# Performance work log

Hardware: AMD Instinct MI355X
Metric: run time of the kernel (lower is better)

The kernel has to match this reference:

```python
import jax, jax.numpy as jnp
import numpy as np


def setup_inputs() -> dict:
    key = jax.random.key(0)
    k_x, k_wih, k_whh, k_bih, k_bhh = jax.random.split(key, 5)
    B, T, F, H = 64, 2048, 256, 512
    s = 1.0 / np.sqrt(H)  # PyTorch RNN default init scale
    return {
        "query": jax.random.normal(k_x, (B, T, F), dtype=jnp.float32),
        "W_ih": jax.random.uniform(k_wih, (H, F), jnp.float32, -s, s),
        "W_hh": jax.random.uniform(k_whh, (H, H), jnp.float32, -s, s),
        "b_ih": jax.random.uniform(k_bih, (H,), jnp.float32, -s, s),
        "b_hh": jax.random.uniform(k_bhh, (H,), jnp.float32, -s, s),
    }


def reference(query, W_ih, W_hh, b_ih, b_hh):
    # Vanilla tanh RNN (batch_first): h_t = tanh(x_t W_ih^T + b_ih + h_{t-1} W_hh^T + b_hh)
    B, T, F = query.shape
    H = W_hh.shape[0]
    # Precompute the input projection for all timesteps as one big GEMM.
    x_proj = jnp.einsum("btf,hf->bth", query, W_ih) + b_ih + b_hh  # [B, T, H]

    def step(h, x_t):
        h_new = jnp.tanh(x_t + h @ W_hh.T)  # [B, H]
        return h_new, h_new

    h0 = jnp.zeros((B, H), dtype=query.dtype)
    h_last, outs = jax.lax.scan(step, h0, jnp.swapaxes(x_proj, 0, 1))  # scan over T
    output = jnp.swapaxes(outs, 0, 1)  # [B, T, H]
    hidden = h_last[None]              # [1, B, H] (num_layers=1)
    return output, hidden
```

## Files before the change

### kernel.cpp

```cpp
#include <hip/hip_runtime.h>
#include <cstdint>

#define B_SZ 64
#define T_SZ 2048
#define F_SZ 256
#define H_SZ 512

typedef _Float16 f16x8 __attribute__((ext_vector_type(8)));
typedef float f32x4 __attribute__((ext_vector_type(4)));

#if defined(__has_builtin)
#if __has_builtin(__builtin_amdgcn_fdot2)
#define HAVE_FDOT2 1
#endif
#endif
#ifndef HAVE_FDOT2
#define HAVE_FDOT2 0
#endif

typedef _Float16 half2v __attribute__((ext_vector_type(2)));
union H2U { uint32_t u; half2v h; _Float16 e[2]; };

__device__ __forceinline__ float fdot2f(uint32_t a, uint32_t b, float c) {
  H2U ua, ub; ua.u = a; ub.u = b;
#if HAVE_FDOT2
  return __builtin_amdgcn_fdot2(ua.h, ub.h, c, false);
#else
  return c + (float)ua.e[0] * (float)ub.e[0] + (float)ua.e[1] * (float)ub.e[1];
#endif
}

__device__ __forceinline__ uint32_t pack2h(float x, float y) {
  H2U v; v.e[0] = (_Float16)x; v.e[1] = (_Float16)y; return v.u;
}

__device__ __forceinline__ float fast_tanh(float x) {
  float xc = fminf(9.0f, fmaxf(-9.0f, x));
  float e = __expf(2.0f * xc);
  return (e - 1.0f) / (e + 1.0f);
}

__device__ __forceinline__ f16x8 pack8(const float* p) {
  float4 v0 = *(const float4*)p;
  float4 v1 = *(const float4*)(p + 4);
  f16x8 a;
  a[0] = (_Float16)v0.x; a[1] = (_Float16)v0.y;
  a[2] = (_Float16)v0.z; a[3] = (_Float16)v0.w;
  a[4] = (_Float16)v1.x; a[5] = (_Float16)v1.y;
  a[6] = (_Float16)v1.z; a[7] = (_Float16)v1.w;
  return a;
}

__device__ __forceinline__ void step_barrier() {
  asm volatile("s_waitcnt lgkmcnt(0)\n\ts_barrier" ::: "memory");
}

__global__ __launch_bounds__(512) void prep_kernel(
    const float* __restrict__ w_hh, uint4* __restrict__ wsf) {
  int idx = blockIdx.x * 512 + threadIdx.x;
  int lane = idx & 63;
  int kt = (idx >> 6) & 15;
  int w = idx >> 10;
  int m = lane & 15, g = lane >> 4;
  const float* p = w_hh + (size_t)(64 * w + 48 + m) * H_SZ + kt * 32 + g * 8;
  f16x8 a = pack8(p);
  wsf[idx] = __builtin_bit_cast(uint4, a);
}

__global__ __launch_bounds__(256) void proj_kernel(
    const float* __restrict__ q, const float* __restrict__ w_ih,
    const float* __restrict__ b_ih, const float* __restrict__ b_hh,
    float* __restrict__ xp) {
  __shared__ uint32_t lds_a[16][128 + 4];
  __shared__ uint32_t lds_b[16][128 + 4];
  const int tid = threadIdx.x;
  const int nt = blockIdx.x & 3;
  const int mt = blockIdx.x >> 2;
  const int m0 = mt * 128, n0 = nt * 128;
  const int tx = tid & 15, ty = tid >> 4;
  const int sr = tid >> 3, sc4 = tid & 7;

  float bias[8];
#pragma unroll
  for (int j = 0; j < 8; ++j) {
    int n = n0 + tx * 8 + j;
    bias[j] = b_ih[n] + b_hh[n];
  }
  float acc[8][8];
#pragma unroll
  for (int i = 0; i < 8; ++i)
#pragma unroll
    for (int j = 0; j < 8; ++j) acc[i][j] = 0.f;

  for (int k0 = 0; k0 < F_SZ; k0 += 32) {
#pragma unroll
    for (int i = 0; i < 4; ++i) {
      int r = sr + 32 * i;
      float4 v = *(const float4*)(q + (size_t)(m0 + r) * F_SZ + k0 + sc4 * 4);
      lds_a[sc4 * 2 + 0][r] = pack2h(v.x, v.y);
      lds_a[sc4 * 2 + 1][r] = pack2h(v.z, v.w);
      float4 w = *(const float4*)(w_ih + (size_t)(n0 + r) * F_SZ + k0 + sc4 * 4);
      lds_b[sc4 * 2 + 0][r] = pack2h(w.x, w.y);
      lds_b[sc4 * 2 + 1][r] = pack2h(w.z, w.w);
    }
    __syncthreads();
#pragma unroll
    for (int kp = 0; kp < 16; ++kp) {
      uint32_t a8[8], b8[8];
#pragma unroll
      for (int i = 0; i < 8; ++i) a8[i] = lds_a[kp][ty * 8 + i];
#pragma unroll
      for (int j = 0; j < 8; ++j) b8[j] = lds_b[kp][tx * 8 + j];
#pragma unroll
      for (int i = 0; i < 8; ++i)
#pragma unroll
        for (int j = 0; j < 8; ++j)
          acc[i][j] = fdot2f(a8[i], b8[j], acc[i][j]);
    }
    __syncthreads();
  }
#pragma unroll
  for (int i = 0; i < 8; ++i) {
    size_t row = (size_t)(m0 + ty * 8 + i);
    float4 o0, o1;
    o0.x = acc[i][0] + bias[0]; o0.y = acc[i][1] + bias[1];
    o0.z = acc[i][2] + bias[2]; o0.w = acc[i][3] + bias[3];
    o1.x = acc[i][4] + bias[4]; o1.y = acc[i][5] + bias[5];
    o1.z = acc[i][6] + bias[6]; o1.w = acc[i][7] + bias[7];
    *(float4*)(xp + row * H_SZ + n0 + tx * 8) = o0;
    *(float4*)(xp + row * H_SZ + n0 + tx * 8 + 4) = o1;
  }
}

__global__ __attribute__((amdgpu_flat_work_group_size(512, 512),
                          amdgpu_waves_per_eu(2, 2)))
void rnn_kernel(const float* __restrict__ w_hh, const uint4* __restrict__ wsf,
                float* __restrict__ out) {
  extern __shared__ char smem[];
  uint4* lds_w = (uint4*)smem;
  _Float16* lds_h = (_Float16*)(smem + 131072);

  const int b = blockIdx.x;
  const int tid = threadIdx.x;
  const int w = tid >> 6;
  const int lane = tid & 63;
  const int m = lane & 15;
  const int g = lane >> 4;

  f16x8 af[2][16];
#pragma unroll
  for (int tile = 0; tile < 2; ++tile) {
    const float* rowp = w_hh + (size_t)(64 * w + tile * 16 + m) * H_SZ;
#pragma unroll
    for (int kt = 0; kt < 16; ++kt)
      af[tile][kt] = pack8(rowp + kt * 32 + g * 8);
  }
  {
    const float* rowp = w_hh + (size_t)(64 * w + 32 + m) * H_SZ;
#pragma unroll
    for (int kt = 0; kt < 16; ++kt) {
      f16x8 a = pack8(rowp + kt * 32 + g * 8);
      lds_w[(w * 16 + kt) * 64 + lane] = __builtin_bit_cast(uint4, a);
    }
  }
  lds_h[tid] = (_Float16)0.f;
  lds_h[512 + tid] = (_Float16)0.f;
  __syncthreads();

  const int row = 64 * w + (m >> 2) * 16 + g * 4 + (m & 3);
  const bool b8 = (m & 8) != 0, b4 = (m & 4) != 0;
  const bool b2 = (m & 2) != 0, b1 = (m & 1) != 0;

  const uint4* swp = wsf + (size_t)(w * 16) * 64 + lane;
  const uint4* lwp = lds_w + (w * 16) * 64 + lane;

  float* outb = out + (size_t)b * T_SZ * H_SZ;
  float xc = outb[row];
  float hlast = 0.f;

#pragma unroll 1
  for (int t = 0; t < T_SZ; ++t) {
    int tn = (t + 1 < T_SZ) ? t + 1 : t;
    float xn = outb[(size_t)tn * H_SZ + row];

    uint4 sf0 = swp[0 * 64],  sf1 = swp[1 * 64],  sf2 = swp[2 * 64],
          sf3 = swp[3 * 64],  sf4 = swp[4 * 64],  sf5 = swp[5 * 64],
          sf6 = swp[6 * 64],  sf7 = swp[7 * 64],  sf8 = swp[8 * 64],
          sf9 = swp[9 * 64],  sf10 = swp[10 * 64], sf11 = swp[11 * 64],
          sf12 = swp[12 * 64], sf13 = swp[13 * 64], sf14 = swp[14 * 64],
          sf15 = swp[15 * 64];

    const _Float16* hb = lds_h + (t & 1) * 512;
    f32x4 c0 = {0.f, 0.f, 0.f, 0.f}, c1 = c0, c2 = c0, c3 = c0;
#define STEP_KT(kt, sfk)                                                      \
    {                                                                         \
      f16x8 bf = *(const f16x8*)(hb + (kt) * 32 + g * 8);                     \
      c0 = __builtin_amdgcn_mfma_f32_16x16x32_f16(af[0][kt], bf, c0, 0, 0, 0);\
      c1 = __builtin_amdgcn_mfma_f32_16x16x32_f16(af[1][kt], bf, c1, 0, 0, 0);\
      uint4 lf = lwp[(kt) * 64];                                              \
      c2 = __builtin_amdgcn_mfma_f32_16x16x32_f16(                            \
          __builtin_bit_cast(f16x8, lf), bf, c2, 0, 0, 0);                    \
      c3 = __builtin_amdgcn_mfma_f32_16x16x32_f16(                            \
          __builtin_bit_cast(f16x8, sfk), bf, c3, 0, 0, 0);                   \
    }
    STEP_KT(0, sf0)   STEP_KT(1, sf1)   STEP_KT(2, sf2)   STEP_KT(3, sf3)
    STEP_KT(4, sf4)   STEP_KT(5, sf5)   STEP_KT(6, sf6)   STEP_KT(7, sf7)
    STEP_KT(8, sf8)   STEP_KT(9, sf9)   STEP_KT(10, sf10) STEP_KT(11, sf11)
    STEP_KT(12, sf12) STEP_KT(13, sf13) STEP_KT(14, sf14) STEP_KT(15, sf15)
#undef STEP_KT

    float p0 = b8 ? (b4 ? c3[0] : c2[0]) : (b4 ? c1[0] : c0[0]);
    float p1 = b8 ? (b4 ? c3[1] : c2[1]) : (b4 ? c1[1] : c0[1]);
    float p2 = b8 ? (b4 ? c3[2] : c2[2]) : (b4 ? c1[2] : c0[2]);
    float p3 = b8 ? (b4 ? c3[3] : c2[3]) : (b4 ? c1[3] : c0[3]);
    float q01 = b1 ? p1 : p0;
    float q23 = b1 ? p3 : p2;
    float v = b2 ? q23 : q01;

    float hnew = fast_tanh(xc + v);
    outb[(size_t)t * H_SZ + row] = hnew;
    lds_h[((t + 1) & 1) * 512 + row] = (_Float16)hnew;
    hlast = hnew;
    xc = xn;
    step_barrier();
  }

  out[(size_t)B_SZ * T_SZ * H_SZ + (size_t)b * H_SZ + row] = hlast;
}

extern "C" void kernel_launch(void* const* d_in, const int* in_sizes, int n_in,
                              void* d_out, int out_size, void* d_ws,
                              size_t ws_size, hipStream_t stream) {
  (void)in_sizes; (void)n_in; (void)out_size; (void)ws_size;
  const float* q    = (const float*)d_in[0];
  const float* w_ih = (const float*)d_in[1];
  const float* w_hh = (const float*)d_in[2];
  const float* b_ih = (const float*)d_in[3];
  const float* b_hh = (const float*)d_in[4];
  float* out = (float*)d_out;
  uint4* wsf = (uint4*)d_ws;

  prep_kernel<<<dim3(16), dim3(512), 0, stream>>>(w_hh, wsf);

  proj_kernel<<<dim3((B_SZ * T_SZ / 128) * (H_SZ / 128)), dim3(256), 0,
                stream>>>(q, w_ih, b_ih, b_hh, out);

  hipFuncSetAttribute(reinterpret_cast<const void*>(rnn_kernel),
                      hipFuncAttributeMaxDynamicSharedMemorySize, 133120);
  rnn_kernel<<<dim3(B_SZ), dim3(512), 133120, stream>>>(w_hh, wsf, out);
}
```

Baseline: 3.387 ms.

## Stream two W_hh tiles from L2 with rotating register prefetch instead of LDS

Moves the third weight tile of W_hh out of LDS so that two of the four 16-row tiles are streamed from a prepacked global workspace each timestep. The streamed fragments go through a four-deep rotating register buffer, with the loads for the next k-slices issued while the current MFMAs run. This removes the large LDS weight staging and its LDS read traffic. In exchange it doubles the per-step global/L2 weight traffic and depends on the prefetch hiding L2 latency.

```diff
diff --git a/kernel.cpp b/kernel.cpp
--- a/kernel.cpp
+++ b/kernel.cpp
@@ -59,10 +59,12 @@
     const float* __restrict__ w_hh, uint4* __restrict__ wsf) {
   int idx = blockIdx.x * 512 + threadIdx.x;
   int lane = idx & 63;
-  int kt = (idx >> 6) & 15;
-  int w = idx >> 10;
+  int tp = (idx >> 6) & 1;
+  int kt = (idx >> 7) & 15;
+  int w = idx >> 11;
   int m = lane & 15, g = lane >> 4;
-  const float* p = w_hh + (size_t)(64 * w + 48 + m) * H_SZ + kt * 32 + g * 8;
+  const float* p =
+      w_hh + (size_t)(64 * w + 32 + 16 * tp + m) * H_SZ + kt * 32 + g * 8;
   f16x8 a = pack8(p);
   wsf[idx] = __builtin_bit_cast(uint4, a);
 }
@@ -137,8 +139,7 @@
 void rnn_kernel(const float* __restrict__ w_hh, const uint4* __restrict__ wsf,
                 float* __restrict__ out) {
   extern __shared__ char smem[];
-  uint4* lds_w = (uint4*)smem;
-  _Float16* lds_h = (_Float16*)(smem + 131072);
+  _Float16* lds_h = (_Float16*)smem;
 
   const int b = blockIdx.x;
   const int tid = threadIdx.x;
@@ -155,14 +156,6 @@
     for (int kt = 0; kt < 16; ++kt)
       af[tile][kt] = pack8(rowp + kt * 32 + g * 8);
   }
-  {
-    const float* rowp = w_hh + (size_t)(64 * w + 32 + m) * H_SZ;
-#pragma unroll
-    for (int kt = 0; kt < 16; ++kt) {
-      f16x8 a = pack8(rowp + kt * 32 + g * 8);
-      lds_w[(w * 16 + kt) * 64 + lane] = __builtin_bit_cast(uint4, a);
-    }
-  }
   lds_h[tid] = (_Float16)0.f;
   lds_h[512 + tid] = (_Float16)0.f;
   __syncthreads();
@@ -171,42 +164,42 @@
   const bool b8 = (m & 8) != 0, b4 = (m & 4) != 0;
   const bool b2 = (m & 2) != 0, b1 = (m & 1) != 0;
 
-  const uint4* swp = wsf + (size_t)(w * 16) * 64 + lane;
-  const uint4* lwp = lds_w + (w * 16) * 64 + lane;
+  const uint4* swp = wsf + (size_t)(w * 32) * 64 + lane;
 
   float* outb = out + (size_t)b * T_SZ * H_SZ;
   float xc = outb[row];
   float hlast = 0.f;
+
+  uint4 rg2[4], rg3[4];
+#pragma unroll
+  for (int k = 0; k < 4; ++k) {
+    rg2[k] = swp[k * 128];
+    rg3[k] = swp[k * 128 + 64];
+  }
 
 #pragma unroll 1
   for (int t = 0; t < T_SZ; ++t) {
     int tn = (t + 1 < T_SZ) ? t + 1 : t;
     float xn = outb[(size_t)tn * H_SZ + row];
 
-    uint4 sf0 = swp[0 * 64],  sf1 = swp[1 * 64],  sf2 = swp[2 * 64],
-          sf3 = swp[3 * 64],  sf4 = swp[4 * 64],  sf5 = swp[5 * 64],
-          sf6 = swp[6 * 64],  sf7 = swp[7 * 64],  sf8 = swp[8 * 64],
-          sf9 = swp[9 * 64],  sf10 = swp[10 * 64], sf11 = swp[11 * 64],
-          sf12 = swp[12 * 64], sf13 = swp[13 * 64], sf14 = swp[14 * 64],
-          sf15 = swp[15 * 64];
-
     const _Float16* hb = lds_h + (t & 1) * 512;
     f32x4 c0 = {0.f, 0.f, 0.f, 0.f}, c1 = c0, c2 = c0, c3 = c0;
-#define STEP_KT(kt, sfk)                                                      \
+#define STEP_KT(kt)                                                           \
     {                                                                         \
       f16x8 bf = *(const f16x8*)(hb + (kt) * 32 + g * 8);                     \
       c0 = __builtin_amdgcn_mfma_f32_16x16x32_f16(af[0][kt], bf, c0, 0, 0, 0);\
       c1 = __builtin_amdgcn_mfma_f32_16x16x32_f16(af[1][kt], bf, c1, 0, 0, 0);\
-      uint4 lf = lwp[(kt) * 64];                                              \
       c2 = __builtin_amdgcn_mfma_f32_16x16x32_f16(                            \
-          __builtin_bit_cast(f16x8, lf), bf, c2, 0, 0, 0);                    \
+          __builtin_bit_cast(f16x8, rg2[(kt) & 3]), bf, c2, 0, 0, 0);         \
       c3 = __builtin_amdgcn_mfma_f32_16x16x32_f16(                            \
-          __builtin_bit_cast(f16x8, sfk), bf, c3, 0, 0, 0);                   \
+          __builtin_bit_cast(f16x8, rg3[(kt) & 3]), bf, c3, 0, 0, 0);         \
+      rg2[(kt) & 3] = swp[(((kt) + 4) & 15) * 128];                           \
+      rg3[(kt) & 3] = swp[(((kt) + 4) & 15) * 128 + 64];                      \
     }
-    STEP_KT(0, sf0)   STEP_KT(1, sf1)   STEP_KT(2, sf2)   STEP_KT(3, sf3)
-    STEP_KT(4, sf4)   STEP_KT(5, sf5)   STEP_KT(6, sf6)   STEP_KT(7, sf7)
-    STEP_KT(8, sf8)   STEP_KT(9, sf9)   STEP_KT(10, sf10) STEP_KT(11, sf11)
-    STEP_KT(12, sf12) STEP_KT(13, sf13) STEP_KT(14, sf14) STEP_KT(15, sf15)
+    STEP_KT(0)  STEP_KT(1)  STEP_KT(2)  STEP_KT(3)
+    STEP_KT(4)  STEP_KT(5)  STEP_KT(6)  STEP_KT(7)
+    STEP_KT(8)  STEP_KT(9)  STEP_KT(10) STEP_KT(11)
+    STEP_KT(12) STEP_KT(13) STEP_KT(14) STEP_KT(15)
 #undef STEP_KT
 
     float p0 = b8 ? (b4 ? c3[0] : c2[0]) : (b4 ? c1[0] : c0[0]);
@@ -240,12 +233,12 @@
   float* out = (float*)d_out;
   uint4* wsf = (uint4*)d_ws;
 
-  prep_kernel<<<dim3(16), dim3(512), 0, stream>>>(w_hh, wsf);
+  prep_kernel<<<dim3(32), dim3(512), 0, stream>>>(w_hh, wsf);
 
   proj_kernel<<<dim3((B_SZ * T_SZ / 128) * (H_SZ / 128)), dim3(256), 0,
                 stream>>>(q, w_ih, b_ih, b_hh, out);
 
   hipFuncSetAttribute(reinterpret_cast<const void*>(rnn_kernel),
-                      hipFuncAttributeMaxDynamicSharedMemorySize, 133120);
-  rnn_kernel<<<dim3(B_SZ), dim3(512), 133120, stream>>>(w_hh, wsf, out);
-}
+                      hipFuncAttributeMaxDynamicSharedMemorySize, 98304);
+  rnn_kernel<<<dim3(B_SZ), dim3(512), 98304, stream>>>(w_hh, wsf, out);
+}
```

Result: slower. 5.874 ms (+73.4%).
